# Optimization experiments

Hardware: AMD Instinct MI355X
Metric: run time of the kernel (lower is better)

The kernel has to match this reference:

```python
import jax, jax.numpy as jnp
import numpy as np

N = 1048576  # total points
B = 64       # number of clouds in batch
D = 64       # feature dim


def _make_lengths():
    rng = np.random.RandomState(0)
    w = rng.rand(B) + 0.5
    lengths = np.floor(w / w.sum() * N).astype(np.int64)
    lengths[-1] += N - lengths.sum()  # make lengths sum exactly to N
    return lengths


def setup_inputs() -> dict:
    key = jax.random.key(0)
    x = jax.random.normal(key, (N, D), dtype=jnp.float32)
    lengths_np = _make_lengths()
    segment_ids = jnp.asarray(np.repeat(np.arange(B, dtype=np.int64), lengths_np))
    lengths = jnp.asarray(lengths_np)
    return {"x": x, "segment_ids": segment_ids, "lengths": lengths}


def reference(x, segment_ids, lengths):
    # fused segmented mean: one pass over x instead of B separate mean kernels
    sums = jax.ops.segment_sum(x, segment_ids, num_segments=B)  # [B, D]
    return sums / lengths.astype(x.dtype)[:, None]
```

## Files before the change

kernel.cpp:

```cpp
#include <hip/hip_runtime.h>


#define D 64
#define ROWS_PER_BLOCK 512
#define NSLOT 4

__global__ __launch_bounds__(256) void seg_sum_kernel(
    const float* __restrict__ x,
    const int*   __restrict__ seg,
    float*       __restrict__ acc,
    int n_rows)
{
    __shared__ float lacc[NSLOT][D];
    __shared__ int   lused[NSLOT];
    __shared__ int   lseg0;

    const int tid = threadIdx.x;
    const int r0  = blockIdx.x * ROWS_PER_BLOCK;
    if (r0 >= n_rows) return;
    int r1 = r0 + ROWS_PER_BLOCK;
    if (r1 > n_rows) r1 = n_rows;

    for (int i = tid; i < NSLOT * D; i += 256) ((float*)lacc)[i] = 0.0f;
    if (tid < NSLOT) lused[tid] = 0;
    if (tid == 0) lseg0 = seg[r0];
    __syncthreads();
    const int seg0 = lseg0;

    const int col     = (tid & 15) * 4;
    const int rowlane = tid >> 4;

    float4 a = make_float4(0.f, 0.f, 0.f, 0.f);
    int cur = seg0;

    for (int r = r0 + rowlane; r < r1; r += 16) {
        const int s = seg[r];
        const float4 v = *(const float4*)(x + (size_t)r * D + col);
        if (s == cur) {
            a.x += v.x; a.y += v.y; a.z += v.z; a.w += v.w;
        } else {
            const int slot = cur - seg0;
            if (slot >= 0 && slot < NSLOT) {
                atomicAdd(&lacc[slot][col + 0], a.x);
                atomicAdd(&lacc[slot][col + 1], a.y);
                atomicAdd(&lacc[slot][col + 2], a.z);
                atomicAdd(&lacc[slot][col + 3], a.w);
                lused[slot] = 1;
            } else {
                atomicAdd(&acc[(size_t)cur * D + col + 0], a.x);
                atomicAdd(&acc[(size_t)cur * D + col + 1], a.y);
                atomicAdd(&acc[(size_t)cur * D + col + 2], a.z);
                atomicAdd(&acc[(size_t)cur * D + col + 3], a.w);
            }
            a = v;
            cur = s;
        }
    }
    {
        const int slot = cur - seg0;
        if (slot >= 0 && slot < NSLOT) {
            atomicAdd(&lacc[slot][col + 0], a.x);
            atomicAdd(&lacc[slot][col + 1], a.y);
            atomicAdd(&lacc[slot][col + 2], a.z);
            atomicAdd(&lacc[slot][col + 3], a.w);
            lused[slot] = 1;
        } else {
            atomicAdd(&acc[(size_t)cur * D + col + 0], a.x);
            atomicAdd(&acc[(size_t)cur * D + col + 1], a.y);
            atomicAdd(&acc[(size_t)cur * D + col + 2], a.z);
            atomicAdd(&acc[(size_t)cur * D + col + 3], a.w);
        }
    }
    __syncthreads();

    for (int i = tid; i < NSLOT * D; i += 256) {
        const int slot = i >> 6;
        const int c    = i & (D - 1);
        if (lused[slot]) {
            atomicAdd(&acc[(size_t)(seg0 + slot) * D + c], lacc[slot][c]);
        }
    }
}

__global__ __launch_bounds__(256) void seg_div_kernel(
    const float* __restrict__ acc,
    const int*   __restrict__ len,
    float*       __restrict__ out,
    int total)
{
    const int i = blockIdx.x * blockDim.x + threadIdx.x;
    if (i < total) {
        out[i] = acc[i] / (float)len[i >> 6];
    }
}

extern "C" void kernel_launch(void* const* d_in, const int* in_sizes, int n_in,
                              void* d_out, int out_size, void* d_ws, size_t ws_size,
                              hipStream_t stream) {
    const float* x   = (const float*)d_in[0];
    const int*   seg = (const int*)d_in[1];
    const int*   len = (const int*)d_in[2];
    float*       out = (float*)d_out;
    float*       acc = (float*)d_ws;

    const int n_rows = in_sizes[1];
    const int B      = in_sizes[2];
    const int total  = B * D;

    hipMemsetAsync(acc, 0, (size_t)total * sizeof(float), stream);

    const int grid1 = (n_rows + ROWS_PER_BLOCK - 1) / ROWS_PER_BLOCK;
    seg_sum_kernel<<<grid1, 256, 0, stream>>>(x, seg, acc, n_rows);

    const int grid2 = (total + 255) / 256;
    seg_div_kernel<<<grid2, 256, 0, stream>>>(acc, len, out, total);
}
```

Baseline: 370.6 us.

## Fuse segment mean into one kernel with last-block division and boundary fast path

```diff
diff --git a/kernel.cpp b/kernel.cpp
--- a/kernel.cpp
+++ b/kernel.cpp
@@ -3,94 +3,116 @@
 
 #define D 64
 #define ROWS_PER_BLOCK 512
-#define NSLOT 4
+#define NTHREADS 256
 
-__global__ __launch_bounds__(256) void seg_sum_kernel(
+typedef float f32x4 __attribute__((ext_vector_type(4)));
+
+__device__ int g_done_counter = 0;
+
+__global__ __launch_bounds__(NTHREADS) void seg_mean_kernel(
     const float* __restrict__ x,
     const int*   __restrict__ seg,
-    float*       __restrict__ acc,
-    int n_rows)
+    const int*   __restrict__ len,
+    float*       __restrict__ out,
+    int n_rows, int total)
 {
-    __shared__ float lacc[NSLOT][D];
-    __shared__ int   lused[NSLOT];
-    __shared__ int   lseg0;
+    __shared__ float lacc[2][D];
+    __shared__ int sBoundary, sNb, sIsLast;
 
     const int tid = threadIdx.x;
     const int r0  = blockIdx.x * ROWS_PER_BLOCK;
-    if (r0 >= n_rows) return;
     int r1 = r0 + ROWS_PER_BLOCK;
     if (r1 > n_rows) r1 = n_rows;
-
-    for (int i = tid; i < NSLOT * D; i += 256) ((float*)lacc)[i] = 0.0f;
-    if (tid < NSLOT) lused[tid] = 0;
-    if (tid == 0) lseg0 = seg[r0];
-    __syncthreads();
-    const int seg0 = lseg0;
 
     const int col     = (tid & 15) * 4;
     const int rowlane = tid >> 4;
 
-    float4 a = make_float4(0.f, 0.f, 0.f, 0.f);
-    int cur = seg0;
+    if (r0 < n_rows) {
+        const int s0 = seg[r0];
+        const int sN = seg[r1 - 1];
 
-    for (int r = r0 + rowlane; r < r1; r += 16) {
-        const int s = seg[r];
-        const float4 v = *(const float4*)(x + (size_t)r * D + col);
-        if (s == cur) {
-            a.x += v.x; a.y += v.y; a.z += v.z; a.w += v.w;
+        for (int i = tid; i < 2 * D; i += NTHREADS) ((float*)lacc)[i] = 0.0f;
+        if (tid == 0) { sBoundary = r1; sNb = 0; }
+        __syncthreads();
+
+        int boundary = r1, nb = 0;
+        if (s0 != sN) {
+            for (int i = r0 + 1 + tid; i < r1; i += NTHREADS) {
+                if (seg[i] != seg[i - 1]) { atomicAdd(&sNb, 1); atomicMin(&sBoundary, i); }
+            }
+            __syncthreads();
+            boundary = sBoundary;
+            nb       = sNb;
+        }
+
+        if (nb <= 1) {
+            f32x4 a0 = {0.f, 0.f, 0.f, 0.f};
+            f32x4 a1 = {0.f, 0.f, 0.f, 0.f};
+            for (int r = r0 + rowlane; r < r1; r += 16) {
+                const f32x4 v = __builtin_nontemporal_load(
+                    reinterpret_cast<const f32x4*>(x + (size_t)r * D + col));
+                if (r < boundary) { a0 += v; } else { a1 += v; }
+            }
+            atomicAdd(&lacc[0][col + 0], a0.x);
+            atomicAdd(&lacc[0][col + 1], a0.y);
+            atomicAdd(&lacc[0][col + 2], a0.z);
+            atomicAdd(&lacc[0][col + 3], a0.w);
+            if (boundary < r1) {
+                atomicAdd(&lacc[1][col + 0], a1.x);
+                atomicAdd(&lacc[1][col + 1], a1.y);
+                atomicAdd(&lacc[1][col + 2], a1.z);
+                atomicAdd(&lacc[1][col + 3], a1.w);
+            }
+            __syncthreads();
+            if (tid < D) {
+                atomicAdd(&out[(size_t)s0 * D + tid], lacc[0][tid]);
+                if (boundary < r1)
+                    atomicAdd(&out[(size_t)sN * D + tid], lacc[1][tid]);
+            }
         } else {
-            const int slot = cur - seg0;
-            if (slot >= 0 && slot < NSLOT) {
-                atomicAdd(&lacc[slot][col + 0], a.x);
-                atomicAdd(&lacc[slot][col + 1], a.y);
-                atomicAdd(&lacc[slot][col + 2], a.z);
-                atomicAdd(&lacc[slot][col + 3], a.w);
-                lused[slot] = 1;
-            } else {
-                atomicAdd(&acc[(size_t)cur * D + col + 0], a.x);
-                atomicAdd(&acc[(size_t)cur * D + col + 1], a.y);
-                atomicAdd(&acc[(size_t)cur * D + col + 2], a.z);
-                atomicAdd(&acc[(size_t)cur * D + col + 3], a.w);
+            f32x4 a = {0.f, 0.f, 0.f, 0.f};
+            int cur = -1;
+            for (int r = r0 + rowlane; r < r1; r += 16) {
+                const int s = seg[r];
+                const f32x4 v = *reinterpret_cast<const f32x4*>(x + (size_t)r * D + col);
+                if (s != cur) {
+                    if (cur >= 0) {
+                        atomicAdd(&out[(size_t)cur * D + col + 0], a.x);
+                        atomicAdd(&out[(size_t)cur * D + col + 1], a.y);
+                        atomicAdd(&out[(size_t)cur * D + col + 2], a.z);
+                        atomicAdd(&out[(size_t)cur * D + col + 3], a.w);
+                    }
+                    a = {0.f, 0.f, 0.f, 0.f};
+                    cur = s;
+                }
+                a += v;
             }
-            a = v;
-            cur = s;
+            if (cur >= 0) {
+                atomicAdd(&out[(size_t)cur * D + col + 0], a.x);
+                atomicAdd(&out[(size_t)cur * D + col + 1], a.y);
+                atomicAdd(&out[(size_t)cur * D + col + 2], a.z);
+                atomicAdd(&out[(size_t)cur * D + col + 3], a.w);
+            }
         }
     }
-    {
-        const int slot = cur - seg0;
-        if (slot >= 0 && slot < NSLOT) {
-            atomicAdd(&lacc[slot][col + 0], a.x);
-            atomicAdd(&lacc[slot][col + 1], a.y);
-            atomicAdd(&lacc[slot][col + 2], a.z);
-            atomicAdd(&lacc[slot][col + 3], a.w);
-            lused[slot] = 1;
-        } else {
-            atomicAdd(&acc[(size_t)cur * D + col + 0], a.x);
-            atomicAdd(&acc[(size_t)cur * D + col + 1], a.y);
-            atomicAdd(&acc[(size_t)cur * D + col + 2], a.z);
-            atomicAdd(&acc[(size_t)cur * D + col + 3], a.w);
-        }
+
+    __threadfence();
+    __syncthreads();
+    if (tid == 0) {
+        const int prev = __hip_atomic_fetch_add(&g_done_counter, 1,
+                             __ATOMIC_ACQ_REL, __HIP_MEMORY_SCOPE_AGENT);
+        sIsLast = (prev == (int)gridDim.x - 1);
     }
     __syncthreads();
-
-    for (int i = tid; i < NSLOT * D; i += 256) {
-        const int slot = i >> 6;
-        const int c    = i & (D - 1);
-        if (lused[slot]) {
-            atomicAdd(&acc[(size_t)(seg0 + slot) * D + c], lacc[slot][c]);
+    if (sIsLast) {
+        if (tid == 0)
+            __hip_atomic_store(&g_done_counter, 0,
+                               __ATOMIC_RELAXED, __HIP_MEMORY_SCOPE_AGENT);
+        for (int i = tid; i < total; i += NTHREADS) {
+            const float v = __hip_atomic_load(&out[i],
+                                __ATOMIC_RELAXED, __HIP_MEMORY_SCOPE_AGENT);
+            out[i] = v / (float)len[i >> 6];
         }
-    }
-}
-
-__global__ __launch_bounds__(256) void seg_div_kernel(
-    const float* __restrict__ acc,
-    const int*   __restrict__ len,
-    float*       __restrict__ out,
-    int total)
-{
-    const int i = blockIdx.x * blockDim.x + threadIdx.x;
-    if (i < total) {
-        out[i] = acc[i] / (float)len[i >> 6];
     }
 }
 
@@ -101,17 +123,13 @@
     const int*   seg = (const int*)d_in[1];
     const int*   len = (const int*)d_in[2];
     float*       out = (float*)d_out;
-    float*       acc = (float*)d_ws;
 
     const int n_rows = in_sizes[1];
     const int B      = in_sizes[2];
     const int total  = B * D;
 
-    hipMemsetAsync(acc, 0, (size_t)total * sizeof(float), stream);
+    hipMemsetAsync(out, 0, (size_t)total * sizeof(float), stream);
 
-    const int grid1 = (n_rows + ROWS_PER_BLOCK - 1) / ROWS_PER_BLOCK;
-    seg_sum_kernel<<<grid1, 256, 0, stream>>>(x, seg, acc, n_rows);
-
-    const int grid2 = (total + 255) / 256;
-    seg_div_kernel<<<grid2, 256, 0, stream>>>(acc, len, out, total);
+    const int grid = (n_rows + ROWS_PER_BLOCK - 1) / ROWS_PER_BLOCK;
+    seg_mean_kernel<<<grid, NTHREADS, 0, stream>>>(x, seg, len, out, n_rows, total);
 }
```

Result: slower. 591.8 us (+59.7%).
